# Performance work log

Measured on AMD Instinct MI355X. Metric: run time of the kernel, lower is better.

## Reference

```python
import jax, jax.numpy as jnp
import numpy as np

N = 1147      # 240 lncRNA + 412 disease + 495 miRNA nodes (hard-coded in source)
HID = 512
NH = 8        # heads
P = 73408     # edges (avg degree ~64)
IN_CH = 512


def _ln(x, eps=1e-5):
    m = x.mean(-1, keepdims=True)
    v = ((x - m) ** 2).mean(-1, keepdims=True)
    return (x - m) * jax.lax.rsqrt(v + eps)


def _seg_softmax_agg(logits, v_src, dst, n):
    # logits: [P, NH], v_src: [P, NH, d]; softmax over incoming edges per dst node
    m = jax.ops.segment_max(logits, dst, num_segments=n)
    m = jnp.where(jnp.isfinite(m), m, 0.0)
    a = jnp.exp(logits - m[dst])
    den = jax.ops.segment_sum(a, dst, num_segments=n)
    w = a / (den[dst] + 1e-9)
    return jax.ops.segment_sum(w[..., None] * v_src, dst, num_segments=n)


def _lap_pe(src, dst, n, k):
    # symmetric normalized Laplacian eigenvector positional encoding
    A = jnp.zeros((n, n), jnp.float32).at[src, dst].set(1.0)
    A = jnp.maximum(A, A.T)
    dinv = jax.lax.rsqrt(jnp.maximum(A.sum(1), 1.0))
    L = jnp.eye(n, dtype=jnp.float32) - dinv[:, None] * A * dinv[None, :]
    _, vecs = jnp.linalg.eigh(L)
    return vecs[:, 1:k + 1]  # drop trivial eigenvector


def _edge_layer(h, e, src, dst, Wq, Wk, Wv, We, Wo, Woe, Wfa, Wfb, Wea, Web):
    n, D = h.shape
    d = D // NH
    scale = 1.0 / np.sqrt(d)
    q = (h @ Wq).reshape(n, NH, d)
    k = (h @ Wk).reshape(n, NH, d)
    v = (h @ Wv).reshape(n, NH, d)
    ep = (e @ We).reshape(-1, NH, d)
    score = k[src] * q[dst] * scale * ep           # [P, NH, d]
    e1 = _ln(e + score.reshape(-1, D) @ Woe)       # edge residual path
    e1 = _ln(e1 + jax.nn.relu(e1 @ Wea) @ Web)
    agg = _seg_softmax_agg(score.sum(-1), v[src], dst, n).reshape(n, D)
    h1 = _ln(h + agg @ Wo)
    h1 = _ln(h1 + jax.nn.relu(h1 @ Wfa) @ Wfb)
    return h1, e1


def _gt_layer(h, src, dst, Wq, Wk, Wv, Wo, Wfa, Wfb):
    n, D = h.shape
    d = D // NH
    scale = 1.0 / np.sqrt(d)
    q = (h @ Wq).reshape(n, NH, d)
    k = (h @ Wk).reshape(n, NH, d)
    v = (h @ Wv).reshape(n, NH, d)
    logits = (k[src] * q[dst]).sum(-1) * scale     # [P, NH]
    agg = _seg_softmax_agg(logits, v[src], dst, n).reshape(n, D)
    h1 = _ln(h + agg @ Wo)
    h1 = _ln(h1 + jax.nn.relu(h1 @ Wfa) @ Wfb)
    return h1


def setup_inputs() -> dict:
    key = jax.random.key(0)
    ks = jax.random.split(key, 32)
    s = 0.02
    w = lambda i, shp: jax.random.normal(ks[i], shp, jnp.float32) * s
    return {
        'H': jax.random.normal(ks[0], (N, 1147), jnp.float32),
        'edge_w': jax.random.uniform(ks[1], (P, 1), jnp.float32),
        'edge_src': jax.random.randint(ks[2], (P,), 0, N, jnp.int32),
        'edge_dst': jax.random.randint(ks[3], (P,), 0, N, jnp.int32),
        'W_lin': w(4, (1147, IN_CH)), 'b_lin': jnp.zeros((IN_CH,), jnp.float32),
        'W_e': w(5, (1, HID)), 'b_e': jnp.zeros((HID,), jnp.float32),
        'W_h': w(6, (IN_CH, HID)), 'b_h': jnp.zeros((HID,), jnp.float32),
        'W_lap': w(7, (HID, HID)), 'b_lap': jnp.zeros((HID,), jnp.float32),
        'Wq1': w(8, (HID, HID)), 'Wk1': w(9, (HID, HID)), 'Wv1': w(10, (HID, HID)),
        'We1': w(11, (HID, HID)), 'Wo1': w(12, (HID, HID)), 'Woe1': w(13, (HID, HID)),
        'Wf1a': w(14, (HID, 2 * HID)), 'Wf1b': w(15, (2 * HID, HID)),
        'We1a': w(16, (HID, 2 * HID)), 'We1b': w(17, (2 * HID, HID)),
        'Wq2': w(18, (HID, HID)), 'Wk2': w(19, (HID, HID)), 'Wv2': w(20, (HID, HID)),
        'Wo2': w(21, (HID, HID)),
        'Wf2a': w(22, (HID, 2 * HID)), 'Wf2b': w(23, (2 * HID, HID)),
    }


def reference(H, edge_w, W_lin, b_lin, W_e, b_e, W_h, b_h, W_lap, b_lap,
              Wq1, Wk1, Wv1, We1, Wo1, Woe1, Wf1a, Wf1b, We1a, We1b,
              Wq2, Wk2, Wv2, Wo2, Wf2a, Wf2b, edge_src, edge_dst):
    e = edge_w @ W_e + b_e                       # embedding_e on edge weights
    h = (H @ W_lin + b_lin) @ W_h + b_h          # linear(1147->in_ch) then embedding_h
    pe = _lap_pe(edge_src, edge_dst, N, HID)     # laplacian positional encoding
    h = h + pe @ W_lap + b_lap
    z, _ = _edge_layer(h, e, edge_src, edge_dst, Wq1, Wk1, Wv1, We1,
                       Wo1, Woe1, Wf1a, Wf1b, We1a, We1b)
    z = _gt_layer(z, edge_src, edge_dst, Wq2, Wk2, Wv2, Wo2, Wf2a, Wf2b)
    return z  # [N, HID], already flat per node
```

## Files before the change

### kernel.cpp

```cpp
#include <hip/hip_runtime.h>
#include <hip/hip_cooperative_groups.h>
#include <math.h>

#define NN 1147
#define HID 512
#define LDAe 1152
#define LDQ 1152
#define LDD 1147
#define EPS32 5.9604644775390625e-08f
#define SAFMIN32 1.17549435e-38f
#define I0E 1026
#define TGRID 256

struct EDMeta { int K; int nrot; int early; float rho; };
struct ETree { int st[64]; int sz[64]; int cnt; };
struct MergeLvl { int cnt; int st[32]; int n1[32]; int n2[32]; };

__device__ __forceinline__ float lapy2f(float x, float y){
  float xa=fabsf(x), ya=fabsf(y), w=fmaxf(xa,ya), z2=fminf(xa,ya);
  if (z2==0.f) return w;
  float q=z2/w; return w*sqrtf(1.f+q*q);
}
__device__ __forceinline__ void slartg(float ff, float gg, float* c, float* s, float* r){
  if (gg==0.f){ *c=1.f; *s=0.f; *r=ff; }
  else if (ff==0.f){ *c=0.f; *s=copysignf(1.f,gg); *r=fabsf(gg); }
  else {
    float d=sqrtf(ff*ff+gg*gg);
    *c=fabsf(ff)/d;
    *r=copysignf(d,ff);
    *s=gg/(*r);
  }
}
__device__ void slaev2(float a, float b, float cc, float* rt1, float* rt2, float* cs1, float* sn1){
  float sm=a+cc, df=a-cc, adf=fabsf(df), tb=b+b, ab=fabsf(tb);
  float acmx, acmn;
  if (fabsf(a)>fabsf(cc)){ acmx=a; acmn=cc; } else { acmx=cc; acmn=a; }
  float rt;
  if (adf>ab) rt=adf*sqrtf(1.f+(ab/adf)*(ab/adf));
  else if (adf<ab) rt=ab*sqrtf(1.f+(adf/ab)*(adf/ab));
  else rt=ab*sqrtf(2.f);
  int sgn1;
  if (sm<0.f){ *rt1=0.5f*(sm-rt); sgn1=-1; *rt2=(acmx/(*rt1))*acmn-(b/(*rt1))*b; }
  else if (sm>0.f){ *rt1=0.5f*(sm+rt); sgn1=1; *rt2=(acmx/(*rt1))*acmn-(b/(*rt1))*b; }
  else { *rt1=0.5f*rt; *rt2=-0.5f*rt; sgn1=1; }
  int sgn2; float cs;
  if (df>=0.f){ cs=df+rt; sgn2=1; } else { cs=df-rt; sgn2=-1; }
  float acs=fabsf(cs);
  if (acs>ab){ float ct=-tb/cs; *sn1=1.f/sqrtf(1.f+ct*ct); *cs1=ct*(*sn1); }
  else {
    if (ab==0.f){ *cs1=1.f; *sn1=0.f; }
    else { float tn=-cs/tb; *cs1=1.f/sqrtf(1.f+tn*tn); *sn1=tn*(*cs1); }
  }
  if (sgn1==sgn2){ float tn=*cs1; *cs1=-(*sn1); *sn1=tn; }
}
__device__ void lamrg0(int n1,int n2,const float* a,int dtrd1,int dtrd2,int* idx){
  int n1sv=n1,n2sv=n2;
  int ind1=(dtrd1>0)?0:(n1-1);
  int ind2=(dtrd2>0)?n1:(n1+n2-1);
  int i=0;
  while(n1sv>0&&n2sv>0){
    if(a[ind1]<=a[ind2]){idx[i++]=ind1;ind1+=dtrd1;n1sv--;}
    else{idx[i++]=ind2;ind2+=dtrd2;n2sv--;}
  }
  while(n2sv>0){idx[i++]=ind2;ind2+=dtrd2;n2sv--;}
  while(n1sv>0){idx[i++]=ind1;ind1+=dtrd1;n1sv--;}
}

__global__ __launch_bounds__(256) void k_zero_f(float* p, int n){
  int i = blockIdx.x*256+threadIdx.x; if (i<n) p[i]=0.f;
}
__global__ __launch_bounds__(256) void k_zero_i(int* p, int n){
  int i = blockIdx.x*256+threadIdx.x; if (i<n) p[i]=0;
}

__global__ __launch_bounds__(256) void k_adj(const int* __restrict__ src, const int* __restrict__ dst,
                                             float* __restrict__ A, int P){
  int p = blockIdx.x*256+threadIdx.x;
  if (p>=P) return;
  int s=src[p], d=dst[p];
  A[(size_t)s*LDAe+d]=1.f;
  A[(size_t)d*LDAe+s]=1.f;
}
__global__ __launch_bounds__(256) void k_deg(const float* __restrict__ A, float* __restrict__ dinv){
  int row=blockIdx.x; int tid=threadIdx.x;
  __shared__ float red[256];
  float s=0.f;
  for (int c=tid;c<NN;c+=256) s+=A[(size_t)row*LDAe+c];
  red[tid]=s; __syncthreads();
  for(int st=128;st;st>>=1){ if(tid<st) red[tid]+=red[tid+st]; __syncthreads(); }
  if(tid==0) dinv[row]=1.f/sqrtf(fmaxf(red[0],1.f));
}
__global__ __launch_bounds__(256) void k_lap(float* __restrict__ A, const float* __restrict__ dinv){
  int row=blockIdx.y; int col=blockIdx.x*256+threadIdx.x;
  if (col>=NN) return;
  size_t idx=(size_t)row*LDAe+col;
  float v=A[idx];
  float v1=(dinv[row]*v)*dinv[col];
  float v2=(dinv[col]*v)*dinv[row];
  A[idx] = ((row==col)?1.f:0.f) - 0.5f*(v1+v2);
}

__device__ __forceinline__ float dload(const float* p){
  return __hip_atomic_load(p, __ATOMIC_RELAXED, __HIP_MEMORY_SCOPE_AGENT);
}
__device__ __forceinline__ void dstore(float* p, float v){
  __hip_atomic_store(p, v, __ATOMIC_RELAXED, __HIP_MEMORY_SCOPE_AGENT);
}

__device__ __forceinline__ void gbar(unsigned* flags, unsigned* gen, unsigned tgt){
  __syncthreads();
  if (threadIdx.x==0)
    __hip_atomic_store(&flags[blockIdx.x], tgt, __ATOMIC_RELAXED, __HIP_MEMORY_SCOPE_AGENT);
  if (blockIdx.x==0){
    while (__hip_atomic_load(&flags[threadIdx.x], __ATOMIC_RELAXED, __HIP_MEMORY_SCOPE_AGENT) < tgt)
      __builtin_amdgcn_s_sleep(2);
    __syncthreads();
    if (threadIdx.x==0)
      __hip_atomic_store(gen, tgt, __ATOMIC_RELAXED, __HIP_MEMORY_SCOPE_AGENT);
  } else {
    if (threadIdx.x==0){
      while (__hip_atomic_load(gen, __ATOMIC_RELAXED, __HIP_MEMORY_SCOPE_AGENT) < tgt)
        __builtin_amdgcn_s_sleep(2);
    }
    __syncthreads();
  }
}

__global__ __launch_bounds__(256) void k_trid(float* __restrict__ A, float* __restrict__ evec,
    float* __restrict__ tauv, float* __restrict__ scalv, float* __restrict__ pv2,
    float* __restrict__ pub4, unsigned* __restrict__ flags, unsigned* __restrict__ gen){
  __shared__ float vbuf[2][1152];
  __shared__ float pcur[1152];
  __shared__ float pubc[1152];
  __shared__ float red[256];
  int tid=threadIdx.x, bid=blockIdx.x;
  int wv=tid>>6, lane=tid&63;
  unsigned tgt=0;
  float tau, scal;
  {
    const float* row0=A;
    int m0=NN-1;
    float s=0.f;
    for(int t=tid;t<m0-1;t+=256){ float x=row0[2+t]; s+=x*x; }
    red[tid]=s; __syncthreads();
    for(int st=128;st;st>>=1){ if(tid<st) red[tid]+=red[tid+st]; __syncthreads(); }
    float alpha=row0[1], xn2=red[0];
    float beta;
    if(xn2==0.f){ tau=0.f; beta=alpha; scal=0.f; }
    else { beta=-copysignf(sqrtf(alpha*alpha+xn2),alpha); tau=(beta-alpha)/beta; scal=1.f/(alpha-beta); }
    if(bid==0&&tid==0){ evec[0]=beta; tauv[0]=tau; scalv[0]=scal; }
    __syncthreads();
    for(int t=tid;t<m0;t+=256) vbuf[0][t]=row0[1+t];
    __syncthreads();
    for(int rr=0;rr<2;rr++){
      int r=4*bid+wv+rr*1024;
      if(r<1||r>=NN) continue;
      const float* arow=A+(size_t)r*LDAe+1;
      float acc=0.f;
      for(int c=lane;c<m0;c+=64){
        float v=(c==0)?1.f:vbuf[0][c]*scal;
        acc+=arow[c]*v;
      }
      for(int o=32;o;o>>=1) acc+=__shfl_down(acc,o,64);
      if(lane==0) dstore(&pv2[r],acc);
    }
    if(bid==0&&wv==1){
      const float* r1=A+(size_t)LDAe;
      for(int c=2+lane;c<NN;c+=64) dstore(&pub4[1280+c],r1[c]);
    }
  }
  gbar(flags,gen,++tgt);
  int cur=0;
  for(int i=0;i<I0E;i++){
    int m=NN-1-i, mp=m-1;
    float* vcur=vbuf[cur]; float* nxt=vbuf[cur^1];
    const float* pvs=pv2+(size_t)(i&1)*1280;
    const float* pbs=pub4+(size_t)((i+1)&3)*1280;
    for(int t=tid;t<m;t+=256){
      pcur[t]=dload(&pvs[(i+1)+t]);
      if(t<mp) pubc[t]=dload(&pbs[(i+2)+t]);
    }
    __syncthreads();
    float s=0.f;
    for(int t=tid;t<m;t+=256){ float v=(t==0)?1.f:vcur[t]*scal; s+=pcur[t]*v; }
    red[tid]=s; __syncthreads();
    for(int st=128;st;st>>=1){ if(tid<st) red[tid]+=red[tid+st]; __syncthreads(); }
    float c2=tau*tau*red[0]*0.5f;
    __syncthreads();
    const float vz=1.f;
    float wR0=tau*pcur[0]-c2*vz;
    for(int t=tid;t<mp;t+=256){
      float vC=vcur[1+t]*scal;
      float wC=tau*pcur[1+t]-c2*vC;
      nxt[t]=pubc[t]-(vz*wC+wR0*vC);
    }
    __syncthreads();
    float s2=0.f;
    for(int t=tid;t<mp-1;t+=256){ float x=nxt[1+t]; s2+=x*x; }
    red[tid]=s2; __syncthreads();
    for(int st=128;st;st>>=1){ if(tid<st) red[tid]+=red[tid+st]; __syncthreads(); }
    float alpha1=nxt[0], xn2=red[0];
    float beta1,tau1,scal1;
    if(xn2==0.f){ tau1=0.f; beta1=alpha1; scal1=0.f; }
    else { beta1=-copysignf(sqrtf(alpha1*alpha1+xn2),alpha1); tau1=(beta1-alpha1)/beta1; scal1=1.f/(alpha1-beta1); }
    if(bid==0&&tid==0){ evec[i+1]=beta1; tauv[i+1]=tau1; scalv[i+1]=scal1; }
    __syncthreads();
    float* pvd=pv2+(size_t)((i+1)&1)*1280;
    float* pbd=pub4+(size_t)((i+2)&3)*1280;
    for(int rr=0;rr<2;rr++){
      int r=4*bid+wv+rr*1024;
      if(r<i+1||r>=NN) continue;
      int tr=r-(i+1);
      float vR=(tr==0)?1.f:vcur[tr]*scal;
      float wR=tau*pcur[tr]-c2*vR;
      float* arow=A+(size_t)r*LDAe;
      if(lane==0) arow[i+1]=arow[i+1]-(vR*wR0+wR*vz);
      if(tr==0){
        for(int c=lane;c<mp;c+=64) arow[i+2+c]=nxt[c];
      } else {
        float acc=0.f;
        int ispub=(tr==1);
        for(int c=lane;c<mp;c+=64){
          float vC=vcur[1+c]*scal;
          float wC=tau*pcur[1+c]-c2*vC;
          float val=arow[i+2+c]-(vR*wC+wR*vC);
          arow[i+2+c]=val;
          float v1=(c==0)?1.f:nxt[c]*scal1;
          acc+=val*v1;
          if(ispub) dstore(&pbd[(i+2)+c],val);
        }
        for(int o=32;o;o>>=1) acc+=__shfl_down(acc,o,64);
        if(lane==0) dstore(&pvd[r],acc);
      }
    }
    gbar(flags,gen,++tgt);
    cur^=1; tau=tau1; scal=scal1;
  }
}
__global__ __launch_bounds__(256) void k_tend(float* __restrict__ A, float* __restrict__ evec,
    float* __restrict__ tauv, float* __restrict__ scalv){
  __shared__ float T[121][122];
  __shared__ float red[256];
  __shared__ float pl[121];
  __shared__ float el[121], tl[121], sl[121];
  __shared__ float sh3[2];
  int tid=threadIdx.x;
  for(int e=tid;e<121*121;e+=256){ int r=e/121,c=e%121; T[r][c]=A[(size_t)(I0E+r)*LDAe + I0E+c]; }
  __syncthreads();
  for(int li=0; li<120; ++li){
    int m=120-li;
    float s=0.f;
    for(int t=tid;t<m-1;t+=256){ float x=T[li][li+2+t]; s+=x*x; }
    red[tid]=s; __syncthreads();
    for(int st=128;st;st>>=1){ if(tid<st) red[tid]+=red[tid+st]; __syncthreads(); }
    if(tid==0){
      float alpha=T[li][li+1], xn2=red[0];
      float beta,tau,scal;
      if(xn2==0.f){ tau=0.f; beta=alpha; scal=0.f; }
      else { beta=-copysignf(sqrtf(alpha*alpha+xn2),alpha); tau=(beta-alpha)/beta; scal=1.f/(alpha-beta); }
      el[li]=beta; tl[li]=tau; sl[li]=scal;
      sh3[0]=tau; sh3[1]=scal;
    }
    __syncthreads();
    float tau=sh3[0], scal=sh3[1];
    if(tid<m){
      float acc=0.f;
      for(int c=0;c<m;c++){
        float v=(c==0)?1.f:T[li][li+1+c]*scal;
        acc+=T[li+1+tid][li+1+c]*v;
      }
      pl[tid]=acc;
    }
    __syncthreads();
    s=0.f;
    for(int t=tid;t<m;t+=256){
      float v=(t==0)?1.f:T[li][li+1+t]*scal;
      s+=pl[t]*v;
    }
    red[tid]=s; __syncthreads();
    for(int st=128;st;st>>=1){ if(tid<st) red[tid]+=red[tid+st]; __syncthreads(); }
    float c2=tau*tau*red[0]*0.5f;
    for(int e=tid;e<m*m;e+=256){
      int r=e/m, c=e%m;
      float vR=(r==0)?1.f:T[li][li+1+r]*scal;
      float vC=(c==0)?1.f:T[li][li+1+c]*scal;
      float wR=tau*pl[r]-c2*vR;
      float wC=tau*pl[c]-c2*vC;
      T[li+1+r][li+1+c]-=vR*wC+wR*vC;
    }
    __syncthreads();
  }
  for(int e=tid;e<121*121;e+=256){ int r=e/121,c=e%121; A[(size_t)(I0E+r)*LDAe + I0E+c]=T[r][c]; }
  for(int t=tid;t<120;t+=256){ evec[I0E+t]=el[t]; tauv[I0E+t]=tl[t]; scalv[I0E+t]=sl[t]; }
}
__global__ __launch_bounds__(256) void k_harvest(const float* __restrict__ A, float* __restrict__ dv){
  int t=blockIdx.x*256+threadIdx.x;
  if (t<NN) dv[t]=A[(size_t)t*LDAe+t];
}

__global__ __launch_bounds__(256) void k_ed_scale(float* __restrict__ D, float* __restrict__ E){
  __shared__ float red[256];
  int tid=threadIdx.x;
  float m=0.f;
  for(int i=tid;i<NN;i+=256) m=fmaxf(m,fabsf(D[i]));
  for(int i=tid;i<NN-1;i+=256) m=fmaxf(m,fabsf(E[i]));
  red[tid]=m; __syncthreads();
  for(int s=128;s;s>>=1){ if(tid<s) red[tid]=fmaxf(red[tid],red[tid+s]); __syncthreads(); }
  float mul=1.f/red[0];
  __syncthreads();
  for(int i=tid;i<NN;i+=256) D[i]*=mul;
  for(int i=tid;i<NN-1;i+=256) E[i]*=mul;
}
__global__ void k_ed_cuts(float* D, const float* E, ETree t){
  int b=threadIdx.x;
  if (b==0||b>=t.cnt) return;
  int cut=t.st[b];
  float ae=fabsf(E[cut-1]);
  D[cut-1]-=ae; D[cut]-=ae;
}

__device__ void steqr1(int n, float* d, float* e, float* z, int ldz){
  if (n<=1) return;
  const float eps=EPS32, eps2=EPS32*EPS32, safmin=SAFMIN32;
  float workc[32], works[32];
  int nmaxit=n*30, jtot=0;
  int l1=0;
  for(;;){
    if (l1>n-1) break;
    if (l1>0) e[l1-1]=0.f;
    int m;
    for(m=l1;m<n-1;m++){
      float tst=fabsf(e[m]);
      if (tst==0.f) break;
      if (tst<=(sqrtf(fabsf(d[m]))*sqrtf(fabsf(d[m+1])))*eps){ e[m]=0.f; break; }
    }
    int l=l1, lend=m, lsv=l, lendsv=lend;
    l1=m+1;
    if (lend==l) continue;
    float anorm=0.f;
    for(int i=l;i<=lend;i++) anorm=fmaxf(anorm,fabsf(d[i]));
    for(int i=l;i<lend;i++) anorm=fmaxf(anorm,fabsf(e[i]));
    if (anorm==0.f) continue;
    if (fabsf(d[lend])<fabsf(d[l])){ lend=lsv; l=lendsv; }
    float c,s,g,r,p,f,b,rt1,rt2;
    if (lend>l){
      for(;;){
        int mm;
        for(mm=l;mm<lend;mm++){
          float tst=e[mm]*e[mm];
          if (tst<=(eps2*fabsf(d[mm]))*fabsf(d[mm+1])+safmin) break;
        }
        if (mm<lend) e[mm]=0.f;
        p=d[l];
        if (mm==l){ d[l]=p; l++; if (l<=lend) continue; else break; }
        if (mm==l+1){
          slaev2(d[l],e[l],d[l+1],&rt1,&rt2,&c,&s);
          for(int row=0;row<n;row++){
            float t1=z[(size_t)(l+1)*ldz+row];
            z[(size_t)(l+1)*ldz+row]=c*t1 - s*z[(size_t)l*ldz+row];
            z[(size_t)l*ldz+row]=s*t1 + c*z[(size_t)l*ldz+row];
          }
          d[l]=rt1; d[l+1]=rt2; e[l]=0.f;
          l+=2;
          if (l<=lend) continue; else break;
        }
        if (jtot==nmaxit) break;
        jtot++;
        g=(d[l+1]-p)/(2.f*e[l]);
        r=lapy2f(g,1.f);
        g=d[mm]-p+(e[l]/(g+copysignf(r,g)));
        s=1.f; c=1.f; p=0.f;
        for(int i=mm-1;i>=l;i--){
          f=s*e[i]; b=c*e[i];
          slartg(g,f,&c,&s,&r);
          if (i!=mm-1) e[i+1]=r;
          g=d[i+1]-p;
          r=(d[i]-g)*s+2.f*c*b;
          p=s*r;
          d[i+1]=g+p;
          g=c*r-b;
          workc[i-l]=c; works[i-l]=-s;
        }
        for(int j2=mm-1;j2>=l;j2--){
          float cc=workc[j2-l], ss2=works[j2-l];
          if (cc!=1.f||ss2!=0.f)
            for(int row=0;row<n;row++){
              float t1=z[(size_t)(j2+1)*ldz+row];
              z[(size_t)(j2+1)*ldz+row]=cc*t1 - ss2*z[(size_t)j2*ldz+row];
              z[(size_t)j2*ldz+row]=ss2*t1 + cc*z[(size_t)j2*ldz+row];
            }
        }
        d[l]=d[l]-p;
        e[l]=g;
      }
    } else {
      for(;;){
        int mm;
        for(mm=l;mm>lend;mm--){
          float tst=e[mm-1]*e[mm-1];
          if (tst<=(eps2*fabsf(d[mm]))*fabsf(d[mm-1])+safmin) break;
        }
        if (mm>lend) e[mm-1]=0.f;
        p=d[l];
        if (mm==l){ d[l]=p; l--; if (l>=lend) continue; else break; }
        if (mm==l-1){
          slaev2(d[l-1],e[l-1],d[l],&rt1,&rt2,&c,&s);
          for(int row=0;row<n;row++){
            float t1=z[(size_t)l*ldz+row];
            z[(size_t)l*ldz+row]=c*t1 - s*z[(size_t)(l-1)*ldz+row];
            z[(size_t)(l-1)*ldz+row]=s*t1 + c*z[(size_t)(l-1)*ldz+row];
          }
          d[l-1]=rt1; d[l]=rt2; e[l-1]=0.f;
          l-=2;
          if (l>=lend) continue; else break;
        }
        if (jtot==nmaxit) break;
        jtot++;
        g=(d[l-1]-p)/(2.f*e[l-1]);
        r=lapy2f(g,1.f);
        g=d[mm]-p+(e[l-1]/(g+copysignf(r,g)));
        s=1.f; c=1.f; p=0.f;
        for(int i=mm;i<=l-1;i++){
          f=s*e[i]; b=c*e[i];
          slartg(g,f,&c,&s,&r);
          if (i!=mm) e[i-1]=r;
          g=d[i]-p;
          r=(d[i+1]-g)*s+2.f*c*b;
          p=s*r;
          d[i]=g+p;
          g=c*r-b;
          workc[i-mm]=c; works[i-mm]=s;
        }
        for(int j2=mm;j2<=l-1;j2++){
          float cc=workc[j2-mm], ss2=works[j2-mm];
          if (cc!=1.f||ss2!=0.f)
            for(int row=0;row<n;row++){
              float t1=z[(size_t)(j2+1)*ldz+row];
              z[(size_t)(j2+1)*ldz+row]=cc*t1 - ss2*z[(size_t)j2*ldz+row];
              z[(size_t)j2*ldz+row]=ss2*t1 + cc*z[(size_t)j2*ldz+row];
            }
        }
        d[l]=d[l]-p;
        e[l-1]=g;
      }
    }
  }
  for(int ii=1;ii<n;ii++){
    int i=ii-1,k=i; float pp=d[i];
    for(int j2=ii;j2<n;j2++) if (d[j2]<pp){k=j2;pp=d[j2];}
    if (k!=i){
      d[k]=d[i]; d[i]=pp;
      for(int row=0;row<n;row++){
        float t1=z[(size_t)i*ldz+row];
        z[(size_t)i*ldz+row]=z[(size_t)k*ldz+row];
        z[(size_t)k*ldz+row]=t1;
      }
    }
  }
}
__global__ void k_ed_leaves(float* D, float* E, float* QM, int* indxq, ETree t){
  int lf=blockIdx.x;
  if (lf>=t.cnt) return;
  int st=t.st[lf], n=t.sz[lf];
  float* z=QM+(size_t)st*LDQ+st;
  for(int c=0;c<n;c++) z[(size_t)c*LDQ+c]=1.f;
  steqr1(n, D+st, E+st, z, LDQ);
  for(int i=0;i<n;i++) indxq[st+i]=i;
}

__global__ __launch_bounds__(256) void k_ed_deflate2(float* __restrict__ D, int* __restrict__ indxq,
    float* __restrict__ dlamda, float* __restrict__ w, float* __restrict__ dstage,
    int* __restrict__ colmap, int* __restrict__ cmtype, int* __restrict__ indxcg,
    int* __restrict__ rotp, int* __restrict__ rotn, float* __restrict__ rotc, float* __restrict__ rots,
    EDMeta* __restrict__ meta, const float* __restrict__ QM, const float* __restrict__ E, MergeLvl lv){
  int mid=blockIdx.x; if(mid>=lv.cnt) return;
  int st=lv.st[mid], n1=lv.n1[mid], n2=lv.n2[mid], n=n1+n2;
  int tid=threadIdx.x;
  __shared__ float zl[1152], dl_[1152], dlam[1152], wl[1152], ds2[1152];
  __shared__ int iq[1152], im[1152], ix[1152], ixp[1152], ict[1152], is2[1152];
  __shared__ float rv[256]; __shared__ int ri[256];
  __shared__ float srho; __shared__ int sK, snrot, searly, simax, sjmax;
  float rr=E[st+n1-1];
  if(tid==0) srho=fabsf(2.f*rr);
  for(int i=tid;i<n;i+=256){
    float v = (i<n1)? QM[(size_t)(st+i)*LDQ + st+n1-1] : QM[(size_t)(st+i)*LDQ + st+n1];
    if(rr<0.f && i>=n1) v=-v;
    zl[i]=v*0.70710678118654752440f;
    dl_[i]=D[st+i];
    int q=indxq[st+i]; if(i>=n1) q+=n1;
    iq[i]=q;
    ict[i]=(i<n1)?1:3;
  }
  __syncthreads();
  {
    float bv=-1.f; int bi=0;
    for(int i2=tid;i2<n;i2+=256){ float a=fabsf(zl[i2]); if(a>bv){bv=a;bi=i2;} }
    rv[tid]=bv; ri[tid]=bi; __syncthreads();
    for(int stp=128;stp;stp>>=1){
      if(tid<stp){ if(rv[tid+stp]>rv[tid]||(rv[tid+stp]==rv[tid]&&ri[tid+stp]<ri[tid])){rv[tid]=rv[tid+stp];ri[tid]=ri[tid+stp];} }
      __syncthreads();
    }
    if(tid==0) simax=ri[0];
    __syncthreads();
  }
  {
    float bv=-1.f; int bi=0;
    for(int i2=tid;i2<n;i2+=256){ float a=fabsf(dl_[i2]); if(a>bv){bv=a;bi=i2;} }
    rv[tid]=bv; ri[tid]=bi; __syncthreads();
    for(int stp=128;stp;stp>>=1){
      if(tid<stp){ if(rv[tid+stp]>rv[tid]||(rv[tid+stp]==rv[tid]&&ri[tid+stp]<ri[tid])){rv[tid]=rv[tid+stp];ri[tid]=ri[tid+stp];} }
      __syncthreads();
    }
    if(tid==0) sjmax=ri[0];
    __syncthreads();
  }
  if(tid==0){
    for(int i=0;i<n;i++) dlam[i]=dl_[iq[i]];
    lamrg0(n1,n2,dlam,1,1,im);
    for(int i=0;i<n;i++) ix[i]=iq[im[i]];
    float tol=8.f*EPS32*fmaxf(fabsf(dl_[sjmax]),fabsf(zl[simax]));
    float rho=srho;
    int K=0,nrot=0,early=0;
    if(rho*fabsf(zl[simax])<=tol){
      early=1;
      for(int i=0;i<n;i++){ int s2=ix[i]; im[i]=s2; iq[i]=2; ds2[i]=dl_[s2]; is2[i]=i; }
    } else {
      int K2=n; int pj=0; int j=0;
      for(;j<n;j++){ int nj=ix[j]; if(rho*fabsf(zl[nj])<=tol){K2--;ict[nj]=4;ixp[K2]=nj;} else {pj=nj;break;} }
      for(j=j+1;;j++){
        if(j>=n) break;
        int nj=ix[j];
        if(rho*fabsf(zl[nj])<=tol){K2--;ict[nj]=4;ixp[K2]=nj;}
        else {
          float s=zl[pj], c=zl[nj];
          float tau2=lapy2f(c,s);
          float t=dl_[nj]-dl_[pj];
          c=c/tau2; s=-s/tau2;
          if(fabsf(t*c*s)<=tol){
            zl[nj]=tau2; zl[pj]=0.f;
            if(ict[nj]!=ict[pj]) ict[nj]=2;
            ict[pj]=4;
            rotp[st+nrot]=pj; rotn[st+nrot]=nj; rotc[st+nrot]=c; rots[st+nrot]=s; nrot++;
            float t2=dl_[pj]*c*c + dl_[nj]*s*s;
            dl_[nj]=dl_[pj]*s*s + dl_[nj]*c*c;
            dl_[pj]=t2;
            K2--;
            int i2=1;
            for(;;){
              if(K2+i2<=n-1 && dl_[pj]<dl_[ixp[K2+i2]]){ ixp[K2+i2-1]=ixp[K2+i2]; ixp[K2+i2]=pj; i2++; }
              else { ixp[K2+i2-1]=pj; break; }
// ... 215 lines not shown
  double ss=0.0;
  for(int i=tid;i<K;i+=256){
    float s=w[st+i]/dcol[i];
    sv[i]=s;
    ss+=(double)s*(double)s;
  }
  red[tid]=ss; __syncthreads();
  for(int st2=128;st2;st2>>=1){ if(tid<st2) red[tid]+=red[tid+st2]; __syncthreads(); }
  float tempf=(float)sqrt(red[0]);
  __syncthreads();
  for(int i=tid;i<K;i+=256) dcol[i]=sv[indxc[i]]/tempf;
}
__global__ __launch_bounds__(256) void k_gemm_cm2(const float* __restrict__ Q2, const float* __restrict__ DC,
    float* __restrict__ QM, const EDMeta* __restrict__ meta, MergeLvl lv){
  int mid=blockIdx.z; if(mid>=lv.cnt) return;
  int st=lv.st[mid], n=lv.n1[mid]+lv.n2[mid];
  int K=meta[mid].K;
  int br=blockIdx.x*64, bj=blockIdx.y*64;
  if (br>=n||bj>=n) return;
  int tid=threadIdx.x, tr=tid/16, tc=tid%16;
  if (bj>=K){
    for(int i=0;i<4;i++){ int r=br+tr*4+i; if(r>=n)continue;
      for(int j2=0;j2<4;j2++){ int cc=bj+tc*4+j2; if(cc>=n)continue;
        QM[(size_t)(st+cc)*LDQ+st+r]=Q2[(size_t)(st+cc)*LDQ+st+r]; } }
    return;
  }
  __shared__ float As[16][65], Bs[16][65];
  float acc[4][4]={};
  for(int k0=0;k0<K;k0+=16){
    for(int l=0;l<4;l++){
      int e2=tid+l*256;
      int rr=e2&63, ii=e2>>6;
      float av=0.f;
      if (br+rr<n && k0+ii<K) av=Q2[(size_t)(st+k0+ii)*LDQ + st+br+rr];
      As[ii][rr]=av;
      int bi=e2&15, bj2=e2>>4;
      float bv=0.f;
      if (k0+bi<K && bj+bj2<n) bv=DC[(size_t)(st+bj+bj2)*LDD + k0+bi];
      Bs[bi][bj2]=bv;
    }
    __syncthreads();
    #pragma unroll
    for(int kk=0;kk<16;kk++){
      float ar[4],br2[4];
      #pragma unroll
      for(int i=0;i<4;i++) ar[i]=As[kk][tr*4+i];
      #pragma unroll
      for(int j2=0;j2<4;j2++) br2[j2]=Bs[kk][tc*4+j2];
      #pragma unroll
      for(int i=0;i<4;i++)
        #pragma unroll
        for(int j2=0;j2<4;j2++) acc[i][j2]+=ar[i]*br2[j2];
    }
    __syncthreads();
  }
  for(int i=0;i<4;i++){
    int r=br+tr*4+i; if (r>=n) continue;
    for(int j2=0;j2<4;j2++){
      int cc=bj+tc*4+j2; if (cc>=n) continue;
      if (cc<K) QM[(size_t)(st+cc)*LDQ + st+r]=acc[i][j2];
      else      QM[(size_t)(st+cc)*LDQ + st+r]=Q2[(size_t)(st+cc)*LDQ + st+r];
    }
  }
}
__global__ void k_ed_post(float* __restrict__ D, const float* __restrict__ dstage,
    int* __restrict__ indxq, const EDMeta* __restrict__ meta, MergeLvl lv){
  int mid=blockIdx.x; if(mid>=lv.cnt||threadIdx.x!=0) return;
  int st=lv.st[mid], n=lv.n1[mid]+lv.n2[mid];
  int K=meta[mid].K;
  float* Ds=D+st; int* ixq=indxq+st;
  for(int i=K;i<n;i++) Ds[i]=dstage[st+i];
  if (meta[mid].early){ for(int i=0;i<n;i++) ixq[i]=i; return; }
  lamrg0(K, n-K, Ds, 1, -1, ixq);
}
__global__ __launch_bounds__(256) void k_ed_gather(const float* __restrict__ QM, const int* __restrict__ indxq,
    float* __restrict__ Vt){
  int row=blockIdx.x*256+threadIdx.x;
  int vec=blockIdx.y;
  if (row>=NN) return;
  int src=indxq[vec+1];
  Vt[(size_t)vec*NN+row]=QM[(size_t)src*LDQ+row];
}

__global__ __launch_bounds__(1024) void k_backt(const float* __restrict__ A, const float* __restrict__ tauv,
                                                const float* __restrict__ scalv, float* __restrict__ Vt){
  int wv=threadIdx.x>>6, lane=threadIdx.x&63;
  int vec=blockIdx.x*16+wv;
  float* col=Vt+(size_t)vec*NN;
  for(int i=NN-2;i>=0;i--){
    float tau=tauv[i];
    if (tau==0.f) continue;
    int m=NN-1-i;
    float scal=scalv[i];
    const float* rowi=A+(size_t)i*LDAe;
    float s=0.f;
    for(int t=lane;t<m;t+=64){
      float v=(t==0)?1.f:rowi[i+1+t]*scal;
      s+=v*col[i+1+t];
    }
    for(int o=32;o;o>>=1) s+=__shfl_down(s,o,64);
    s=__shfl(s,0,64);
    s*=tau;
    for(int t=lane;t<m;t+=64){
      float v=(t==0)?1.f:rowi[i+1+t]*scal;
      col[i+1+t]-=s*v;
    }
  }
}

__global__ __launch_bounds__(256) void k_transpose(const float* __restrict__ in, float* __restrict__ outp){
  __shared__ float tile[32][33];
  int c0=blockIdx.x*32, r0=blockIdx.y*32;
  int tx=threadIdx.x%32, ty=threadIdx.x/32;
  for(int s=0;s<32;s+=8){
    int r=r0+ty+s, c=c0+tx;
    tile[ty+s][tx]=(r<512 && c<NN)? in[(size_t)r*NN+c] : 0.f;
  }
  __syncthreads();
  for(int s=0;s<32;s+=8){
    int r=c0+ty+s, c=r0+tx;
    if (r<NN && c<512) outp[(size_t)r*512+c]=tile[tx][ty+s];
  }
}

__global__ __launch_bounds__(256) void k_gemm(const float* __restrict__ A, const float* __restrict__ B,
    const float* __restrict__ bias, const float* __restrict__ add, float* __restrict__ C,
    int M, int Nc, int K, int relu){
  __shared__ float As[16][65];
  __shared__ float Bs[16][65];
  int bm=blockIdx.y*64, bn=blockIdx.x*64;
  int tid=threadIdx.x;
  int tr=tid/16, tc=tid%16;
  float acc[4][4]={};
  for(int k0=0;k0<K;k0+=16){
    for(int l=0;l<4;l++){
      int e2=tid+l*256;
      int m_=e2/16, kk=e2%16;
      float av=0.f;
      if (bm+m_<M && k0+kk<K) av=A[(size_t)(bm+m_)*K + k0+kk];
      As[kk][m_]=av;
      int k2=e2/64, n2=e2%64;
      float bv=0.f;
      if (k0+k2<K && bn+n2<Nc) bv=B[(size_t)(k0+k2)*Nc + bn+n2];
      Bs[k2][n2]=bv;
    }
    __syncthreads();
    for(int kk=0;kk<16;kk++){
      float ar[4], br[4];
      #pragma unroll
      for(int i=0;i<4;i++) ar[i]=As[kk][tr*4+i];
      #pragma unroll
      for(int j=0;j<4;j++) br[j]=Bs[kk][tc*4+j];
      #pragma unroll
      for(int i=0;i<4;i++)
        #pragma unroll
        for(int j=0;j<4;j++) acc[i][j]+=ar[i]*br[j];
    }
    __syncthreads();
  }
  for(int i=0;i<4;i++){
    int r=bm+tr*4+i;
    if (r>=M) continue;
    for(int j=0;j<4;j++){
      int c=bn+tc*4+j;
      if (c>=Nc) continue;
      float x=acc[i][j];
      if (bias) x+=bias[c];
      if (add)  x+=add[(size_t)r*Nc+c];
      if (relu) x=fmaxf(x,0.f);
      C[(size_t)r*Nc+c]=x;
// ... 159 lines not shown
  const int*   esrc   = (const int*)d_in[2];
  const int*   edst   = (const int*)d_in[3];
  const float* W_lin  = (const float*)d_in[4];
  const float* b_lin  = (const float*)d_in[5];
  const float* W_e    = (const float*)d_in[6];
  const float* b_e    = (const float*)d_in[7];
  const float* W_h    = (const float*)d_in[8];
  const float* b_h    = (const float*)d_in[9];
  const float* W_lap  = (const float*)d_in[10];
  const float* b_lap  = (const float*)d_in[11];
  const float* Wq1    = (const float*)d_in[12];
  const float* Wk1    = (const float*)d_in[13];
  const float* Wv1    = (const float*)d_in[14];
  const float* We1    = (const float*)d_in[15];
  const float* Wo1    = (const float*)d_in[16];
  const float* Wf1a   = (const float*)d_in[18];
  const float* Wf1b   = (const float*)d_in[19];
  const float* Wq2    = (const float*)d_in[22];
  const float* Wk2    = (const float*)d_in[23];
  const float* Wv2    = (const float*)d_in[24];
  const float* Wo2    = (const float*)d_in[25];
  const float* Wf2a   = (const float*)d_in[26];
  const float* Wf2b   = (const float*)d_in[27];
  const int P = in_sizes[1];
  float* out = (float*)d_out;

  char* base=(char*)d_ws;
  size_t off=0;
  auto AF=[&](size_t n)->float*{ float* r=(float*)(base+off); off+=((n*4+255)/256)*256; return r; };
  auto AI=[&](size_t n)->int*{ int* r=(int*)(base+off); off+=((n*4+255)/256)*256; return r; };
  const size_t SLOT=(size_t)NN*HID;
  float* A   = AF((size_t)NN*LDAe);
  float* QM  = AF((size_t)LDQ*NN);
  float* Q2  = AF((size_t)LDQ*NN);
  float* DC  = AF((size_t)LDD*LDD);
  float* dvec  = AF(1280);
  float* evec  = AF(1280);
  float* tauv  = AF(1280);
  float* scalv = AF(1280);
  float* pvec  = AF(1280);
  float* eddl  = AF(1280);
  float* edw   = AF(1280);
  float* edds  = AF(1280);
  float* rotc  = AF(1280);
  float* rots  = AF(1280);
  float* ub    = AF(512);
  float* w1b   = AF(512);
  float* pv2   = AF(2*1280);
  float* pub4  = AF(4*1280);
  int* indxq=AI(1280); int* edcm=AI(1280); int* edcmt=AI(1280); int* edic=AI(1280);
  int* rotp=AI(1280); int* rotn=AI(1280);
  EDMeta* meta=(EDMeta*)AI(192);
  int* icnt=AI(NN); int* iptr=AI(NN+1); int* iidx=AI(P);
  int* barws=AI(512);
  unsigned* flags=(unsigned*)barws;
  unsigned* gen=(unsigned*)(barws+256);
  (void)ws_size; (void)n_in; (void)out_size;

  float* W0=A;        float* W1=A+SLOT;
  float* W2=QM;       float* W3=QM+SLOT;
  float* W4=Q2;       float* W5=Q2+SLOT;
  float* W6=DC;       float* W7=DC+SLOT;
  (void)W7;
  float* Vt=W6;
  float* pe=W2;

  auto GEMM=[&](const float*Am,const float*Bm,const float*bias,const float*add,float*C,int M,int Nc,int K,int relu){
    dim3 g((Nc+63)/64,(M+63)/64);
    k_gemm<<<g,256,0,stream>>>(Am,Bm,bias,add,C,M,Nc,K,relu);
  };

  {
    int ntot=NN*LDAe;
    k_zero_f<<<(ntot+255)/256,256,0,stream>>>(A,ntot);
    k_adj<<<(P+255)/256,256,0,stream>>>(esrc,edst,A,P);
    k_deg<<<NN,256,0,stream>>>(A,pvec);
    dim3 g((NN+255)/256,NN);
    k_lap<<<g,256,0,stream>>>(A,pvec);
  }
  k_zero_i<<<2,256,0,stream>>>(barws,512);
  {
    void* kargs[] = { (void*)&A, (void*)&evec, (void*)&tauv, (void*)&scalv,
                      (void*)&pv2, (void*)&pub4, (void*)&flags, (void*)&gen };
    hipLaunchCooperativeKernel((const void*)k_trid, dim3(TGRID), dim3(256), kargs, 0, stream);
  }
  k_tend<<<1,256,0,stream>>>(A,evec,tauv,scalv);
  k_harvest<<<(NN+255)/256,256,0,stream>>>(A,dvec);

  ETree tr;
  {
    int tmp[64]; tmp[0]=NN; int cnt=1;
    while (tmp[cnt-1]>25){
      for(int j2=cnt-1;j2>=0;j2--){ int p=tmp[j2]; tmp[2*j2]=p/2; tmp[2*j2+1]=p-p/2; }
      cnt*=2;
    }
    tr.cnt=cnt;
    int acc=0;
    for(int j2=0;j2<cnt;j2++){ tr.st[j2]=acc; tr.sz[j2]=tmp[j2]; acc+=tmp[j2]; }
  }
  k_ed_scale<<<1,256,0,stream>>>(dvec,evec);
  k_zero_f<<<(LDQ*NN+255)/256,256,0,stream>>>(QM,LDQ*NN);
  k_ed_cuts<<<1,64,0,stream>>>(dvec,evec,tr);
  k_ed_leaves<<<tr.cnt,1,0,stream>>>(dvec,evec,QM,indxq,tr);

  {
    int csz[64], cst[64], cn=tr.cnt;
    for(int i=0;i<cn;i++){ csz[i]=tr.sz[i]; cst[i]=tr.st[i]; }
    while (cn>1){
      MergeLvl lv; lv.cnt=cn/2;
      int maxn=0;
      for(int i=0;i<cn/2;i++){
        lv.st[i]=cst[2*i]; lv.n1[i]=csz[2*i]; lv.n2[i]=csz[2*i+1];
        int n=lv.n1[i]+lv.n2[i]; if(n>maxn) maxn=n;
      }
      k_ed_deflate2<<<lv.cnt,256,0,stream>>>(dvec,indxq,eddl,edw,edds,edcm,edcmt,edic,
                                             rotp,rotn,rotc,rots,meta,QM,evec,lv);
      { dim3 gr((maxn+255)/256,lv.cnt);
        k_ed_rot2<<<gr,256,0,stream>>>(QM,rotp,rotn,rotc,rots,meta,lv); }
      { dim3 gp((maxn+255)/256,maxn,lv.cnt);
        k_ed_permute<<<gp,256,0,stream>>>(QM,Q2,edcm,edcmt,lv); }
      { dim3 gs((maxn+63)/64,lv.cnt);
        k_ed_secular<<<gs,64,0,stream>>>(eddl,edw,meta,dvec,DC,lv);
        k_ed_lowner<<<gs,64,0,stream>>>(eddl,edw,DC,meta,lv); }
      { dim3 gv(maxn,lv.cnt);
        k_ed_vecs<<<gv,256,0,stream>>>(edw,DC,edic,meta,lv); }
      { dim3 gg((maxn+63)/64,(maxn+63)/64,lv.cnt);
        k_gemm_cm2<<<gg,256,0,stream>>>(Q2,DC,QM,meta,lv); }
      k_ed_post<<<lv.cnt,1,0,stream>>>(dvec,edds,indxq,meta,lv);
      for(int i=0;i<cn/2;i++){ cst[i]=cst[2*i]; csz[i]=csz[2*i]+csz[2*i+1]; }
      cn>>=1;
    }
  }
  { dim3 gg((NN+255)/256,512); k_ed_gather<<<gg,256,0,stream>>>(QM,indxq,Vt); }
  k_backt<<<32,1024,0,stream>>>(A,tauv,scalv,Vt);
  { dim3 g((NN+31)/32,(512+31)/32); k_transpose<<<g,256,0,stream>>>(Vt,pe); }

  float* hx=W0; float* h0=W1; float* hb=W4;
  GEMM(H,W_lin,b_lin,nullptr,hx,NN,HID,NN,0);
  GEMM(hx,W_h,b_h,nullptr,h0,NN,HID,HID,0);
  GEMM(pe,W_lap,b_lap,h0,hb,NN,HID,HID,0);
  k_prep_uw<<<2,256,0,stream>>>(W_e,b_e,We1,ub,w1b);
  k_zero_i<<<(NN+255)/256,256,0,stream>>>(icnt,NN);
  k_count<<<(P+255)/256,256,0,stream>>>(edst,icnt,P);
  k_scan<<<1,1,0,stream>>>(icnt,iptr);
  k_fill<<<NN,256,0,stream>>>(edst,iptr,iidx,P);
  float* qb=W0; float* kb=W1; float* vb=W3;
  GEMM(hb,Wq1,nullptr,nullptr,qb,NN,HID,HID,0);
  GEMM(hb,Wk1,nullptr,nullptr,kb,NN,HID,HID,0);
  GEMM(hb,Wv1,nullptr,nullptr,vb,NN,HID,HID,0);
  float* logit=W2;
  k_elogits<<<(P+3)/4,256,0,stream>>>(qb,kb,esrc,edst,edge_w,ub,w1b,logit,P,1);
  float* wght=W5;
  k_softmax<<<NN,256,0,stream>>>(logit,iptr,iidx,wght);
  float* aggb=W6;
  k_agg<<<NN,512,0,stream>>>(wght,vb,esrc,iptr,iidx,aggb);
  float* ob=W0;
  GEMM(aggb,Wo1,nullptr,nullptr,ob,NN,HID,HID,0);
  float* h1a=W3;
  k_lnadd<<<NN,256,0,stream>>>(hb,ob,h1a);
  float* tb1=W0;
  GEMM(h1a,Wf1a,nullptr,nullptr,tb1,NN,1024,HID,1);
  float* fb=W2;
  GEMM(tb1,Wf1b,nullptr,nullptr,fb,NN,HID,1024,0);
  float* h1=W5;
  k_lnadd<<<NN,256,0,stream>>>(h1a,fb,h1);
  float* q2=W0; float* k2=W1; float* v2=W2;
  GEMM(h1,Wq2,nullptr,nullptr,q2,NN,HID,HID,0);
  GEMM(h1,Wk2,nullptr,nullptr,k2,NN,HID,HID,0);
  GEMM(h1,Wv2,nullptr,nullptr,v2,NN,HID,HID,0);
  float* logit2=W3;
  k_elogits<<<(P+3)/4,256,0,stream>>>(q2,k2,esrc,edst,nullptr,nullptr,nullptr,logit2,P,0);
  float* wght2=W4;
  k_softmax<<<NN,256,0,stream>>>(logit2,iptr,iidx,wght2);
  float* agg2=W6;
  k_agg<<<NN,512,0,stream>>>(wght2,v2,esrc,iptr,iidx,agg2);
  float* o2=W0;
  GEMM(agg2,Wo2,nullptr,nullptr,o2,NN,HID,HID,0);
  float* h2a=W1;
  k_lnadd<<<NN,256,0,stream>>>(h1,o2,h2a);
  float* tb2=W2;
  GEMM(h2a,Wf2a,nullptr,nullptr,tb2,NN,1024,HID,1);
  float* f2=W0;
  GEMM(tb2,Wf2b,nullptr,nullptr,f2,NN,HID,1024,0);
  k_lnadd<<<NN,256,0,stream>>>(h2a,f2,out);
}
```

Before: 32.33 ms.

## Shrink tridiagonalization grid, parallelize leaf QR across lanes, reshape back-transform

The cooperative tridiagonalization kernel now runs 64 blocks of 1024 threads instead of 256 blocks of 256 threads. Each of its roughly thousand grid-wide barriers therefore waits on fewer blocks, and the barrier spin uses a shorter sleep. The divide-and-conquer leaf eigen-solver used to run a single thread per leaf; it now uses a 64-lane wavefront that splits the Givens rotation updates of the eigenvector matrix across lanes, while the scalar recurrence is computed redundantly on every lane. The back-transform kernel moves from 32 blocks of 1024 threads to 128 blocks of 256 threads, and this trades per-block occupancy for more blocks.

After: 30.63 ms. 5.2% less time.

```diff
diff --git a/kernel.cpp b/kernel.cpp
--- a/kernel.cpp
+++ b/kernel.cpp
@@ -10,7 +10,8 @@
 #define EPS32 5.9604644775390625e-08f
 #define SAFMIN32 1.17549435e-38f
 #define I0E 1026
-#define TGRID 256
+#define TGRID 64
+#define TBLK 1024
 
 struct EDMeta { int K; int nrot; int early; float rho; };
 struct ETree { int st[64]; int sz[64]; int cnt; };
@@ -112,21 +113,23 @@
   if (threadIdx.x==0)
     __hip_atomic_store(&flags[blockIdx.x], tgt, __ATOMIC_RELAXED, __HIP_MEMORY_SCOPE_AGENT);
   if (blockIdx.x==0){
-    while (__hip_atomic_load(&flags[threadIdx.x], __ATOMIC_RELAXED, __HIP_MEMORY_SCOPE_AGENT) < tgt)
-      __builtin_amdgcn_s_sleep(2);
+    if (threadIdx.x<TGRID){
+      while (__hip_atomic_load(&flags[threadIdx.x], __ATOMIC_RELAXED, __HIP_MEMORY_SCOPE_AGENT) < tgt)
+        __builtin_amdgcn_s_sleep(1);
+    }
     __syncthreads();
     if (threadIdx.x==0)
       __hip_atomic_store(gen, tgt, __ATOMIC_RELAXED, __HIP_MEMORY_SCOPE_AGENT);
   } else {
     if (threadIdx.x==0){
       while (__hip_atomic_load(gen, __ATOMIC_RELAXED, __HIP_MEMORY_SCOPE_AGENT) < tgt)
-        __builtin_amdgcn_s_sleep(2);
-    }
-    __syncthreads();
-  }
-}
-
-__global__ __launch_bounds__(256) void k_trid(float* __restrict__ A, float* __restrict__ evec,
+        __builtin_amdgcn_s_sleep(1);
+    }
+    __syncthreads();
+  }
+}
+
+__global__ __launch_bounds__(1024) void k_trid(float* __restrict__ A, float* __restrict__ evec,
     float* __restrict__ tauv, float* __restrict__ scalv, float* __restrict__ pv2,
     float* __restrict__ pub4, unsigned* __restrict__ flags, unsigned* __restrict__ gen){
   __shared__ float vbuf[2][1152];
@@ -140,9 +143,12 @@
   {
     const float* row0=A;
     int m0=NN-1;
-    float s=0.f;
-    for(int t=tid;t<m0-1;t+=256){ float x=row0[2+t]; s+=x*x; }
-    red[tid]=s; __syncthreads();
+    if (tid<256){
+      float s=0.f;
+      for(int t=tid;t<m0-1;t+=256){ float x=row0[2+t]; s+=x*x; }
+      red[tid]=s;
+    }
+    __syncthreads();
     for(int st=128;st;st>>=1){ if(tid<st) red[tid]+=red[tid+st]; __syncthreads(); }
     float alpha=row0[1], xn2=red[0];
     float beta;
@@ -150,10 +156,10 @@
     else { beta=-copysignf(sqrtf(alpha*alpha+xn2),alpha); tau=(beta-alpha)/beta; scal=1.f/(alpha-beta); }
     if(bid==0&&tid==0){ evec[0]=beta; tauv[0]=tau; scalv[0]=scal; }
     __syncthreads();
-    for(int t=tid;t<m0;t+=256) vbuf[0][t]=row0[1+t];
+    for(int t=tid;t<m0;t+=TBLK) vbuf[0][t]=row0[1+t];
     __syncthreads();
     for(int rr=0;rr<2;rr++){
-      int r=4*bid+wv+rr*1024;
+      int r=16*bid+wv+rr*1024;
       if(r<1||r>=NN) continue;
       const float* arow=A+(size_t)r*LDAe+1;
       float acc=0.f;
@@ -176,28 +182,34 @@
     float* vcur=vbuf[cur]; float* nxt=vbuf[cur^1];
     const float* pvs=pv2+(size_t)(i&1)*1280;
     const float* pbs=pub4+(size_t)((i+1)&3)*1280;
-    for(int t=tid;t<m;t+=256){
+    for(int t=tid;t<m;t+=TBLK){
       pcur[t]=dload(&pvs[(i+1)+t]);
       if(t<mp) pubc[t]=dload(&pbs[(i+2)+t]);
     }
     __syncthreads();
-    float s=0.f;
-    for(int t=tid;t<m;t+=256){ float v=(t==0)?1.f:vcur[t]*scal; s+=pcur[t]*v; }
-    red[tid]=s; __syncthreads();
+    if (tid<256){
+      float s=0.f;
+      for(int t=tid;t<m;t+=256){ float v=(t==0)?1.f:vcur[t]*scal; s+=pcur[t]*v; }
+      red[tid]=s;
+    }
+    __syncthreads();
     for(int st=128;st;st>>=1){ if(tid<st) red[tid]+=red[tid+st]; __syncthreads(); }
     float c2=tau*tau*red[0]*0.5f;
     __syncthreads();
     const float vz=1.f;
     float wR0=tau*pcur[0]-c2*vz;
-    for(int t=tid;t<mp;t+=256){
+    for(int t=tid;t<mp;t+=TBLK){
       float vC=vcur[1+t]*scal;
       float wC=tau*pcur[1+t]-c2*vC;
       nxt[t]=pubc[t]-(vz*wC+wR0*vC);
     }
     __syncthreads();
-    float s2=0.f;
-    for(int t=tid;t<mp-1;t+=256){ float x=nxt[1+t]; s2+=x*x; }
-    red[tid]=s2; __syncthreads();
+    if (tid<256){
+      float s2=0.f;
+      for(int t=tid;t<mp-1;t+=256){ float x=nxt[1+t]; s2+=x*x; }
+      red[tid]=s2;
+    }
+    __syncthreads();
     for(int st=128;st;st>>=1){ if(tid<st) red[tid]+=red[tid+st]; __syncthreads(); }
     float alpha1=nxt[0], xn2=red[0];
     float beta1,tau1,scal1;
@@ -208,7 +220,7 @@
     float* pvd=pv2+(size_t)((i+1)&1)*1280;
     float* pbd=pub4+(size_t)((i+2)&3)*1280;
     for(int rr=0;rr<2;rr++){
-      int r=4*bid+wv+rr*1024;
+      int r=16*bid+wv+rr*1024;
       if(r<i+1||r>=NN) continue;
       int tr=r-(i+1);
       float vR=(tr==0)?1.f:vcur[tr]*scal;
@@ -319,7 +331,7 @@
   D[cut-1]-=ae; D[cut]-=ae;
 }
 
-__device__ void steqr1(int n, float* d, float* e, float* z, int ldz){
+__device__ void steqr1w(int n, float* d, float* e, float* z, int ldz, int lane){
   if (n<=1) return;
   const float eps=EPS32, eps2=EPS32*EPS32, safmin=SAFMIN32;
   float workc[32], works[32];
@@ -355,7 +367,7 @@
         if (mm==l){ d[l]=p; l++; if (l<=lend) continue; else break; }
         if (mm==l+1){
           slaev2(d[l],e[l],d[l+1],&rt1,&rt2,&c,&s);
-          for(int row=0;row<n;row++){
+          for(int row=lane;row<n;row+=64){
             float t1=z[(size_t)(l+1)*ldz+row];
             z[(size_t)(l+1)*ldz+row]=c*t1 - s*z[(size_t)l*ldz+row];
             z[(size_t)l*ldz+row]=s*t1 + c*z[(size_t)l*ldz+row];
@@ -384,7 +396,7 @@
         for(int j2=mm-1;j2>=l;j2--){
           float cc=workc[j2-l], ss2=works[j2-l];
           if (cc!=1.f||ss2!=0.f)
-            for(int row=0;row<n;row++){
+            for(int row=lane;row<n;row+=64){
               float t1=z[(size_t)(j2+1)*ldz+row];
               z[(size_t)(j2+1)*ldz+row]=cc*t1 - ss2*z[(size_t)j2*ldz+row];
               z[(size_t)j2*ldz+row]=ss2*t1 + cc*z[(size_t)j2*ldz+row];
@@ -405,7 +417,7 @@
         if (mm==l){ d[l]=p; l--; if (l>=lend) continue; else break; }
         if (mm==l-1){
           slaev2(d[l-1],e[l-1],d[l],&rt1,&rt2,&c,&s);
-          for(int row=0;row<n;row++){
+          for(int row=lane;row<n;row+=64){
             float t1=z[(size_t)l*ldz+row];
             z[(size_t)l*ldz+row]=c*t1 - s*z[(size_t)(l-1)*ldz+row];
             z[(size_t)(l-1)*ldz+row]=s*t1 + c*z[(size_t)(l-1)*ldz+row];
@@ -434,7 +446,7 @@
         for(int j2=mm;j2<=l-1;j2++){
           float cc=workc[j2-mm], ss2=works[j2-mm];
           if (cc!=1.f||ss2!=0.f)
-            for(int row=0;row<n;row++){
+            for(int row=lane;row<n;row+=64){
               float t1=z[(size_t)(j2+1)*ldz+row];
               z[(size_t)(j2+1)*ldz+row]=cc*t1 - ss2*z[(size_t)j2*ldz+row];
               z[(size_t)j2*ldz+row]=ss2*t1 + cc*z[(size_t)j2*ldz+row];
@@ -450,7 +462,7 @@
     for(int j2=ii;j2<n;j2++) if (d[j2]<pp){k=j2;pp=d[j2];}
     if (k!=i){
       d[k]=d[i]; d[i]=pp;
-      for(int row=0;row<n;row++){
+      for(int row=lane;row<n;row+=64){
         float t1=z[(size_t)i*ldz+row];
         z[(size_t)i*ldz+row]=z[(size_t)k*ldz+row];
         z[(size_t)k*ldz+row]=t1;
@@ -458,14 +470,15 @@
     }
   }
 }
-__global__ void k_ed_leaves(float* D, float* E, float* QM, int* indxq, ETree t){
+__global__ __launch_bounds__(64) void k_ed_leaves(float* D, float* E, float* QM, int* indxq, ETree t){
   int lf=blockIdx.x;
   if (lf>=t.cnt) return;
+  int lane=threadIdx.x;
   int st=t.st[lf], n=t.sz[lf];
   float* z=QM+(size_t)st*LDQ+st;
-  for(int c=0;c<n;c++) z[(size_t)c*LDQ+c]=1.f;
-  steqr1(n, D+st, E+st, z, LDQ);
-  for(int i=0;i<n;i++) indxq[st+i]=i;
+  for(int c=lane;c<n;c+=64) z[(size_t)c*LDQ+c]=1.f;
+  steqr1w(n, D+st, E+st, z, LDQ, lane);
+  for(int i=lane;i<n;i+=64) indxq[st+i]=i;
 }
 
 __global__ __launch_bounds__(256) void k_ed_deflate2(float* __restrict__ D, int* __restrict__ indxq,
@@ -847,10 +860,10 @@
   Vt[(size_t)vec*NN+row]=QM[(size_t)src*LDQ+row];
 }
 
-__global__ __launch_bounds__(1024) void k_backt(const float* __restrict__ A, const float* __restrict__ tauv,
-                                                const float* __restrict__ scalv, float* __restrict__ Vt){
+__global__ __launch_bounds__(256) void k_backt(const float* __restrict__ A, const float* __restrict__ tauv,
+                                               const float* __restrict__ scalv, float* __restrict__ Vt){
   int wv=threadIdx.x>>6, lane=threadIdx.x&63;
-  int vec=blockIdx.x*16+wv;
+  int vec=blockIdx.x*4+wv;
   float* col=Vt+(size_t)vec*NN;
   for(int i=NN-2;i>=0;i--){
     float tau=tauv[i];
@@ -1176,7 +1189,7 @@
   {
     void* kargs[] = { (void*)&A, (void*)&evec, (void*)&tauv, (void*)&scalv,
                       (void*)&pv2, (void*)&pub4, (void*)&flags, (void*)&gen };
-    hipLaunchCooperativeKernel((const void*)k_trid, dim3(TGRID), dim3(256), kargs, 0, stream);
+    hipLaunchCooperativeKernel((const void*)k_trid, dim3(TGRID), dim3(TBLK), kargs, 0, stream);
   }
   k_tend<<<1,256,0,stream>>>(A,evec,tauv,scalv);
   k_harvest<<<(NN+255)/256,256,0,stream>>>(A,dvec);
@@ -1195,7 +1208,7 @@
   k_ed_scale<<<1,256,0,stream>>>(dvec,evec);
   k_zero_f<<<(LDQ*NN+255)/256,256,0,stream>>>(QM,LDQ*NN);
   k_ed_cuts<<<1,64,0,stream>>>(dvec,evec,tr);
-  k_ed_leaves<<<tr.cnt,1,0,stream>>>(dvec,evec,QM,indxq,tr);
+  k_ed_leaves<<<tr.cnt,64,0,stream>>>(dvec,evec,QM,indxq,tr);
 
   {
     int csz[64], cst[64], cn=tr.cnt;
@@ -1226,7 +1239,7 @@
     }
   }
   { dim3 gg((NN+255)/256,512); k_ed_gather<<<gg,256,0,stream>>>(QM,indxq,Vt); }
-  k_backt<<<32,1024,0,stream>>>(A,tauv,scalv,Vt);
+  k_backt<<<128,256,0,stream>>>(A,tauv,scalv,Vt);
   { dim3 g((NN+31)/32,(512+31)/32); k_transpose<<<g,256,0,stream>>>(Vt,pe); }
 
   float* hx=W0; float* h0=W1; float* hb=W4;
```
